# Performance work log

Hardware: AMD Instinct MI355X
Metric: run time of the kernel (lower is better)

The kernel has to match this reference:

```python
import jax, jax.numpy as jnp
import numpy as np

_SIGMA = 1.5
_K1 = 0.01
_K2 = 0.03
WINDOW_SIZE = 11
VALUE_RANGE = 1.0


def gaussian_window(size: int, sigma: float) -> jnp.ndarray:
    # 1D gaussian, normalized; 2D window is the outer product (sums to 1)
    coords = jnp.arange(size, dtype=jnp.float32) - (size - 1) / 2.0
    g = jnp.exp(-(coords ** 2) / (2.0 * sigma ** 2))
    g = g / g.sum()
    return jnp.outer(g, g)  # (k, k)


def depthwise_conv(img, win2d):
    # img: (N, C, H, W), win2d: (k, k); depthwise valid conv, groups=C
    C = img.shape[1]
    kern = jnp.broadcast_to(win2d[:, :, None, None], win2d.shape + (1, C))  # HWIO
    return jax.lax.conv_general_dilated(
        img, kern, window_strides=(1, 1), padding='VALID',
        dimension_numbers=('NCHW', 'HWIO', 'NCHW'), feature_group_count=C)


def setup_inputs() -> dict:
    key = jax.random.key(0)
    k1, k2 = jax.random.split(key)
    x = jax.random.uniform(k1, (16, 3, 512, 512), dtype=jnp.float32)
    y = jax.random.uniform(k2, (16, 3, 512, 512), dtype=jnp.float32)
    window = gaussian_window(WINDOW_SIZE, _SIGMA)
    return {'x': x, 'y': y, 'window': window}


def reference(x, y, window):
    mu_x = depthwise_conv(x, window)
    mu_y = depthwise_conv(y, window)
    mu_x_sq = mu_x ** 2
    mu_y_sq = mu_y ** 2
    mu_xy = mu_x * mu_y
    sigma_x_sq = depthwise_conv(x * x, window) - mu_x_sq
    sigma_y_sq = depthwise_conv(y * y, window) - mu_y_sq
    sigma_xy = depthwise_conv(x * y, window) - mu_xy
    c1 = (_K1 * VALUE_RANGE) ** 2
    c2 = (_K2 * VALUE_RANGE) ** 2
    cs_map = (2.0 * sigma_xy + c2) / (sigma_x_sq + sigma_y_sq + c2)
    ssim_map = (2.0 * mu_xy + c1) / (mu_x_sq + mu_y_sq + c1) * cs_map
    # mean over spatial dims -> (N, C), mean over channels -> (N,), reduction='mean' -> scalar
    return ssim_map.mean(axis=(-1, -2)).mean(axis=-1).mean()
```

## Files before the change

### kernel.cpp

```cpp
#include <hip/hip_runtime.h>
#include <math.h>

#define KS    11
#define H     512
#define W     512
#define OH    502
#define OW    502
#define NPLANES 48
#define TOTAL_OUT (NPLANES * OH * OW)

#define TH      4
#define IROWS   (TH + KS - 1)
#define NSIG    4
#define LVW     523
#define NTHREADS 512
#define CHUNK   32
#define NCHUNKS 16

__global__ void zero_out_kernel(float* out) { out[0] = 0.0f; }

__device__ __forceinline__ float uniform_f(float v) {
    return __int_as_float(__builtin_amdgcn_readfirstlane(__float_as_int(v)));
}

__global__ __launch_bounds__(NTHREADS, 3) void ssim_kernel(
    const float* __restrict__ x,
    const float* __restrict__ y,
    const float* __restrict__ win,
    float* __restrict__ out)
{
    __shared__ float v[NSIG][TH][LVW];
    __shared__ float w1s[KS];
    __shared__ float wsum[NTHREADS / 64];

    const int t     = threadIdx.x;
    const int chunk = blockIdx.x;
    const int plane = blockIdx.y;

    const int row_lo = chunk * CHUNK;
    const int row_hi = (row_lo + CHUNK < OH) ? (row_lo + CHUNK) : OH;
    const int niter  = (row_hi - row_lo + TH - 1) / TH;

    const float* __restrict__ xp = x + (size_t)plane * (H * W);
    const float* __restrict__ yp = y + (size_t)plane * (H * W);

    if (t < KS) w1s[t] = sqrtf(win[t * KS + t]);
    __syncthreads();

    float w[KS];
#pragma unroll
    for (int k = 0; k < KS; k++) w[k] = uniform_f(w1s[k]);

    const int r  = t & 3;
    const int c0 = (t >> 2) << 2;
    const float c1 = 1e-4f;
    const float c2 = 9e-4f;
    float acc = 0.f;

    float rx[IROWS], ry[IROWS];
#pragma unroll
    for (int j = 0; j < IROWS; j++) {
        int gy = row_lo + j; gy = (gy < H - 1) ? gy : (H - 1);
        rx[j] = xp[gy * W + t];
        ry[j] = yp[gy * W + t];
    }

    for (int it = 0; it < niter; ++it) {
        const int gy0 = row_lo + it * TH;

        float a0[TH], a1[TH], a2[TH], a3[TH];
#pragma unroll
        for (int q = 0; q < TH; q++) { a0[q]=0.f; a1[q]=0.f; a2[q]=0.f; a3[q]=0.f; }

#pragma unroll
        for (int j = 0; j < IROWS; j++) {
            const float xv = rx[j], yv = ry[j];
            const float pss = xv * xv + yv * yv;
            const float pxy = xv * yv;
#pragma unroll
            for (int q = 0; q < TH; q++) {
                if (j - q >= 0 && j - q < KS) {
                    const float wk = w[j - q];
                    a0[q] += wk * xv;
                    a1[q] += wk * yv;
                    a2[q] += wk * pss;
                    a3[q] += wk * pxy;
                }
            }
        }

        __syncthreads();
#pragma unroll
        for (int q = 0; q < TH; q++) {
            v[0][q][t] = a0[q];
            v[1][q][t] = a1[q];
            v[2][q][t] = a2[q];
            v[3][q][t] = a3[q];
        }
        __syncthreads();

        if (it + 1 < niter) {
#pragma unroll
            for (int j = 0; j < IROWS - TH; j++) {
                rx[j] = rx[j + TH];
                ry[j] = ry[j + TH];
            }
#pragma unroll
            for (int j = 0; j < TH; j++) {
                int gy = gy0 + IROWS + j;
                gy = (gy < H - 1) ? gy : (H - 1);
                rx[IROWS - TH + j] = xp[gy * W + t];
                ry[IROWS - TH + j] = yp[gy * W + t];
            }
        }

        float mu[NSIG][TH];
#pragma unroll
        for (int s = 0; s < NSIG; s++) {
            const float* __restrict__ vrow = &v[s][r][c0];
            float vs[IROWS];
#pragma unroll
            for (int j = 0; j < IROWS; j++) vs[j] = vrow[j];
#pragma unroll
            for (int p = 0; p < TH; p++) {
                float m = 0.f;
#pragma unroll
                for (int k = 0; k < KS; k++) m += w[k] * vs[p + k];
                mu[s][p] = m;
            }
        }

        const int grow  = gy0 + r;
        const bool rowok = (grow < row_hi);
#pragma unroll
        for (int p = 0; p < TH; p++) {
            if (rowok && (c0 + p) < OW) {
                const float mux = mu[0][p], muy = mu[1][p];
                const float mxy = mux * muy;
                const float m2  = mux * mux + muy * muy;
                const float sss = mu[2][p] - m2;
                const float sxy = mu[3][p] - mxy;
                const float num = (2.f * sxy + c2) * (2.f * mxy + c1);
                const float den = (sss + c2) * (m2 + c1);
                acc += num * __builtin_amdgcn_rcpf(den);
            }
        }
    }

#pragma unroll
    for (int off = 32; off > 0; off >>= 1)
        acc += __shfl_down(acc, off, 64);

    if ((t & 63) == 0) wsum[t >> 6] = acc;
    __syncthreads();
    if (t == 0) {
        float s = 0.f;
#pragma unroll
        for (int i = 0; i < NTHREADS / 64; i++) s += wsum[i];
        atomicAdd(out, s * (1.0f / (float)TOTAL_OUT));
    }
}

extern "C" void kernel_launch(void* const* d_in, const int* in_sizes, int n_in,
                              void* d_out, int out_size, void* d_ws, size_t ws_size,
                              hipStream_t stream)
{
    const float* x   = (const float*)d_in[0];
    const float* y   = (const float*)d_in[1];
    const float* win = (const float*)d_in[2];
    float* out = (float*)d_out;

    zero_out_kernel<<<1, 1, 0, stream>>>(out);

    dim3 grid(NCHUNKS, NPLANES);
    ssim_kernel<<<grid, NTHREADS, 0, stream>>>(x, y, win, out);
}
```

Baseline: 153.1 us.

## Split each row chunk into two column tiles with halo recompute

Each block now covers half the image width with 256 threads instead of the full width with 512, which doubles the grid and raises the declared occupancy target. The left tile has 10 extra threads that recompute the vertical-pass halo columns so the horizontal pass can read past the tile edge. The aim is more blocks for better load balance and latency hiding across CUs, at the cost of redundant halo loads and compute done serially by a few lanes of one wave.

```diff
diff --git a/kernel.cpp b/kernel.cpp
--- a/kernel.cpp
+++ b/kernel.cpp
@@ -12,8 +12,9 @@
 #define TH      4
 #define IROWS   (TH + KS - 1)
 #define NSIG    4
-#define LVW     523
-#define NTHREADS 512
+#define HALO    10
+#define LVW     267
+#define NTHREADS 256
 #define CHUNK   32
 #define NCHUNKS 16
 
@@ -23,7 +24,7 @@
     return __int_as_float(__builtin_amdgcn_readfirstlane(__float_as_int(v)));
 }
 
-__global__ __launch_bounds__(NTHREADS, 3) void ssim_kernel(
+__global__ __launch_bounds__(NTHREADS, 6) void ssim_kernel(
     const float* __restrict__ x,
     const float* __restrict__ y,
     const float* __restrict__ win,
@@ -34,8 +35,12 @@
     __shared__ float wsum[NTHREADS / 64];
 
     const int t     = threadIdx.x;
-    const int chunk = blockIdx.x;
+    const int tile  = blockIdx.x & 1;
+    const int chunk = blockIdx.x >> 1;
     const int plane = blockIdx.y;
+
+    const int in_base = tile << 8;
+    const int tile_w  = tile ? (OW - 256) : 256;
 
     const int row_lo = chunk * CHUNK;
     const int row_hi = (row_lo + CHUNK < OH) ? (row_lo + CHUNK) : OH;
@@ -57,12 +62,14 @@
     const float c2 = 9e-4f;
     float acc = 0.f;
 
+    const int gx = in_base + t;
+
     float rx[IROWS], ry[IROWS];
 #pragma unroll
     for (int j = 0; j < IROWS; j++) {
         int gy = row_lo + j; gy = (gy < H - 1) ? gy : (H - 1);
-        rx[j] = xp[gy * W + t];
-        ry[j] = yp[gy * W + t];
+        rx[j] = xp[gy * W + gx];
+        ry[j] = yp[gy * W + gx];
     }
 
     for (int it = 0; it < niter; ++it) {
@@ -97,6 +104,43 @@
             v[2][q][t] = a2[q];
             v[3][q][t] = a3[q];
         }
+
+        if (tile == 0 && t < HALO) {
+            const int gxb = 256 + t;
+            float b0[TH], b1[TH], b2[TH], b3[TH];
+#pragma unroll
+            for (int q = 0; q < TH; q++) { b0[q]=0.f; b1[q]=0.f; b2[q]=0.f; b3[q]=0.f; }
+            float hx[IROWS], hy[IROWS];
+#pragma unroll
+            for (int j = 0; j < IROWS; j++) {
+                int gy = gy0 + j; gy = (gy < H - 1) ? gy : (H - 1);
+                hx[j] = xp[gy * W + gxb];
+                hy[j] = yp[gy * W + gxb];
+            }
+#pragma unroll
+            for (int j = 0; j < IROWS; j++) {
+                const float xv = hx[j], yv = hy[j];
+                const float pss = xv * xv + yv * yv;
+                const float pxy = xv * yv;
+#pragma unroll
+                for (int q = 0; q < TH; q++) {
+                    if (j - q >= 0 && j - q < KS) {
+                        const float wk = w[j - q];
+                        b0[q] += wk * xv;
+                        b1[q] += wk * yv;
+                        b2[q] += wk * pss;
+                        b3[q] += wk * pxy;
+                    }
+                }
+            }
+#pragma unroll
+            for (int q = 0; q < TH; q++) {
+                v[0][q][256 + t] = b0[q];
+                v[1][q][256 + t] = b1[q];
+                v[2][q][256 + t] = b2[q];
+                v[3][q][256 + t] = b3[q];
+            }
+        }
         __syncthreads();
 
         if (it + 1 < niter) {
@@ -109,8 +153,8 @@
             for (int j = 0; j < TH; j++) {
                 int gy = gy0 + IROWS + j;
                 gy = (gy < H - 1) ? gy : (H - 1);
-                rx[IROWS - TH + j] = xp[gy * W + t];
-                ry[IROWS - TH + j] = yp[gy * W + t];
+                rx[IROWS - TH + j] = xp[gy * W + gx];
+                ry[IROWS - TH + j] = yp[gy * W + gx];
             }
         }
 
@@ -134,7 +178,7 @@
         const bool rowok = (grow < row_hi);
 #pragma unroll
         for (int p = 0; p < TH; p++) {
-            if (rowok && (c0 + p) < OW) {
+            if (rowok && (c0 + p) < tile_w) {
                 const float mux = mu[0][p], muy = mu[1][p];
                 const float mxy = mux * muy;
                 const float m2  = mux * mux + muy * muy;
@@ -172,6 +216,6 @@
 
     zero_out_kernel<<<1, 1, 0, stream>>>(out);
 
-    dim3 grid(NCHUNKS, NPLANES);
+    dim3 grid(2 * NCHUNKS, NPLANES);
     ssim_kernel<<<grid, NTHREADS, 0, stream>>>(x, y, win, out);
 }
```

New measurement: 208.0 us. 35.9% more time.
